# Performance work log

Measured on AMD Instinct MI355X. Metric: run time of the kernel, lower is better.

The kernel has to match this reference:

```python
import jax, jax.numpy as jnp
import numpy as np

V, D, H, DA, A, S = 50000, 512, 512, 128, 3, 512
MAXS = 8  # max stack depth reached by the generated action sequence
N_ACT = 768


def _lstm(x, h, c, Wih, Whh, bih, bhh):
    # torch.nn.LSTMCell math (batch of 1, vectors of shape (H,))
    z = Wih @ x + bih + Whh @ h + bhh
    i, f, g, o = jnp.split(z, 4)
    i = jax.nn.sigmoid(i); f = jax.nn.sigmoid(f); o = jax.nn.sigmoid(o)
    g = jnp.tanh(g)
    c2 = f * c + i * g
    return o * jnp.tanh(c2), c2


def _forward(sentence, actions, word_embeds, action_embeds, relation_embeds,
             empty_emb, h0, c0, Wih5, Whh5, bih5, bhh5,
             Wih_a, Whh_a, bih_a, bhh_a, W1, b1, W2, b2, We, be):
    # cell ids: 0=buffer 1=stack 2=output 3=entity_fwd 4=entity_bwd
    cell = lambda i, x, h, c: _lstm(x, h, c, Wih5[i], Whh5[i], bih5[i], bhh5[i])
    we = word_embeds[sentence]                      # (S, D) token reps (dropout = identity, eval)
    # buffer StackRNN: tokens pushed in reverse; precompute all buffer states once
    def bstep(hc, x):
        h2, c2 = cell(0, x, hc[0], hc[1])
        return (h2, c2), h2
    _, Hb = jax.lax.scan(bstep, (h0, c0), we[::-1])
    Hbuf = jnp.concatenate([h0[None], Hb], 0)       # (S+1, H); Hbuf[p] = top-of-buffer h at pointer p
    Hs = jnp.zeros((MAXS + 1, H), we.dtype).at[0].set(h0)
    Cs = jnp.zeros((MAXS + 1, H), we.dtype).at[0].set(c0)
    Tk = jnp.zeros((MAXS + 1, D), we.dtype)         # token stored with each stack entry

    def step(carry, a):
        pb, ps, po, pa, Hs, Cs, Tk, ho, co, ha, ca = carry
        buf_e = jnp.where(pb > 0, Hbuf[pb], empty_emb)
        stk_e = jnp.where(ps > 0, Hs[ps], empty_emb)
        out_e = jnp.where(po > 0, ho, empty_emb)
        act_e = jnp.where(pa > 0, ha, empty_emb)
        feat = jnp.concatenate([stk_e, buf_e, out_e, act_e])  # (4H,)
        logits = W2 @ jnp.tanh(W1 @ feat + b1) + b2           # (A,)
        nll = -jax.nn.log_softmax(logits)[a]
        tok_b = we[jnp.clip(S - pb, 0, S - 1)]                # top-of-buffer token
        # SHIFT candidate: push buffer token onto stack LSTM
        hs2, cs2 = cell(1, tok_b, Hs[ps], Cs[ps])
        # OUT candidate: push buffer token onto output LSTM
        ho_o, co_o = cell(2, tok_b, ho, co)
        # REDUCE candidate: pop stack entry, run entity fwd/bwd cells, compose, push to output
        tok_s = Tk[ps]
        ehf, _ = cell(3, tok_s, h0, c0)
        ehb, _ = cell(4, tok_s, h0, c0)
        ent = jnp.tanh(We @ jnp.concatenate([ehf, ehb, relation_embeds[a]]) + be)
        ho_r, co_r = cell(2, ent, ho, co)
        sh = a == 0; ot = a == 1; rd = a == 2
        w = jnp.clip(ps + 1, 0, MAXS)
        Hs = Hs.at[w].set(jnp.where(sh, hs2, Hs[w]))
        Cs = Cs.at[w].set(jnp.where(sh, cs2, Cs[w]))
        Tk = Tk.at[w].set(jnp.where(sh, tok_b, Tk[w]))
        ho = jnp.where(ot, ho_o, jnp.where(rd, ho_r, ho))
        co = jnp.where(ot, co_o, jnp.where(rd, co_r, co))
        ha, ca = _lstm(action_embeds[a], ha, ca, Wih_a, Whh_a, bih_a, bhh_a)
        pb = pb - jnp.where(sh | ot, 1, 0)
        ps = ps + jnp.where(sh, 1, 0) - jnp.where(rd, 1, 0)
        po = po + jnp.where(ot | rd, 1, 0)
        pa = pa + 1
        return (pb, ps, po, pa, Hs, Cs, Tk, ho, co, ha, ca), nll

    init = (jnp.int32(S), jnp.int32(0), jnp.int32(0), jnp.int32(0),
            Hs, Cs, Tk, h0, c0, h0, c0)
    _, nlls = jax.lax.scan(step, init, actions)
    return nlls  # (N_ACT,) per-action negative log-likelihoods


def setup_inputs() -> dict:
    key = jax.random.key(0)
    ks = jax.random.split(key, 24)
    f = lambda k, shp: jax.random.normal(k, shp, dtype=jnp.float32) * 0.05
    sentence = jax.random.randint(ks[0], (S,), 1, V, dtype=jnp.int32)
    # valid transition sequence: even token -> OUT; odd token -> SHIFT then REDUCE
    acts = []
    for i in range(S):
        acts += [1] if i % 2 == 0 else [0, 2]
    actions = jnp.asarray(np.array(acts, dtype=np.int32))
    return dict(
        sentence=sentence, actions=actions,
        word_embeds=f(ks[1], (V, D)),
        action_embeds=f(ks[2], (A, DA)),
        relation_embeds=f(ks[3], (A, DA)),
        empty_emb=f(ks[4], (H,)), h0=f(ks[5], (H,)), c0=f(ks[6], (H,)),
        Wih5=f(ks[7], (5, 4 * H, D)), Whh5=f(ks[8], (5, 4 * H, H)),
        bih5=f(ks[9], (5, 4 * H)), bhh5=f(ks[10], (5, 4 * H)),
        Wih_a=f(ks[11], (4 * H, DA)), Whh_a=f(ks[12], (4 * H, H)),
        bih_a=f(ks[13], (4 * H,)), bhh_a=f(ks[14], (4 * H,)),
        W1=f(ks[15], (H, 4 * H)), b1=f(ks[16], (H,)),
        W2=f(ks[17], (A, H)), b2=f(ks[18], (A,)),
        We=f(ks[19], (D, 2 * H + DA)), be=f(ks[20], (D,)))


def reference(sentence, actions, word_embeds, action_embeds, relation_embeds,
              empty_emb, h0, c0, Wih5, Whh5, bih5, bhh5,
              Wih_a, Whh_a, bih_a, bhh_a, W1, b1, W2, b2, We, be):
    return _forward(sentence, actions, word_embeds, action_embeds, relation_embeds,
                    empty_emb, h0, c0, Wih5, Whh5, bih5, bhh5,
                    Wih_a, Whh_a, bih_a, bhh_a, W1, b1, W2, b2, We, be)
```

## Files before the change

kernel.cpp:

```cpp
#include <hip/hip_runtime.h>
#include <math.h>

#define H 512
#define D 512
#define DA 128
#define MAXS 8
#define GH 2048
#define SFIX 512
#define NFIX 768
#define WPC 16
#define CANARY 0x7FC00BADu

typedef unsigned short ushort_t;

__device__ __forceinline__ float b2f(ushort_t v) {
  return __uint_as_float(((unsigned int)v) << 16);
}
__device__ __forceinline__ float sigm_f(float x) {
  return 1.f / (1.f + __expf(-x));
}
__device__ __forceinline__ float tanh_f(float x) {
  return 1.f - 2.f / (1.f + __expf(2.f * x));
}

__device__ int   g_dtype;
__device__ float g_Wih5[5 * GH * D];
__device__ float g_WihA[GH * DA];
__device__ float g_W1[H * GH];
__device__ float g_We[H * (2 * H + DA)];
__device__ float g_W2[3 * H];
__device__ float g_aemb[3 * DA];
__device__ float g_remb[3 * DA];
__device__ float g_empty[H];
__device__ float g_h0[H];
__device__ float g_c0[H];
__device__ float g_b1[H];
__device__ float g_be[D];
__device__ float g_b2[4];
__device__ float g_bih5[5 * GH];
__device__ float g_bhh5[5 * GH];
__device__ float g_bihA[GH];
__device__ float g_bhhA[GH];
__device__ int g_bidx_xb[SFIX];
__device__ int g_bsh[NFIX], g_csh[NFIX], g_par[NFIX], g_map_s[NFIX];
__device__ int g_bot[NFIX], g_cot[NFIX];
__device__ int g_bre[NFIX], g_cre[NFIX], g_map_o[NFIX];
__device__ int g_btok[NFIX], g_cide[NFIX], g_redact[NFIX];
__device__ int g_bufp[NFIX], g_stksrc[NFIX], g_outsrc[NFIX];
__device__ int g_counts[16];
__device__ float g_we[SFIX * D];
__device__ float g_cb[6 * GH];
__device__ float g_Pa[3 * GH];
__device__ float g_XB[SFIX * GH];
__device__ float g_Xso[NFIX * GH];
__device__ float g_E[NFIX * GH];
__device__ float g_E2[NFIX * GH];
__device__ float g_Bent[NFIX * 1152];
__device__ float g_ent[NFIX * H];
__device__ float g_Hbuf[(SFIX + 1) * H];
__device__ float g_Sh[NFIX * H], g_Sc[NFIX * H];
__device__ float g_Hos[NFIX * H], g_Has[NFIX * H];
__device__ float g_feat[NFIX * GH];
__device__ float g_t1[NFIX * H];

__device__ __forceinline__ float* f_conv(int s) {
  switch (s) {
    case 0: return g_Wih5;  case 1: return g_WihA;  case 2: return g_W1;
    case 3: return g_We;    case 4: return g_W2;    case 5: return g_aemb;
    case 6: return g_remb;  case 7: return g_empty; case 8: return g_h0;
    case 9: return g_c0;    case 10: return g_b1;   case 11: return g_be;
    case 12: return g_b2;   case 13: return g_bih5; case 14: return g_bhh5;
    case 15: return g_bihA; case 16: return g_bhhA;
    default: return nullptr;
  }
}
__device__ __forceinline__ const float* f_amat(int s) {
  switch (s) {
    case 0: return g_Wih5; case 1: return g_WihA;
    case 2: return g_We;   case 3: return g_W1;
    default: return nullptr;
  }
}
__device__ __forceinline__ const float* f_src(int s) {
  switch (s) {
    case 0: return g_we;   case 1: return g_ent; case 2: return g_Bent;
    case 3: return g_feat; case 4: return g_aemb;
    default: return nullptr;
  }
}
__device__ __forceinline__ float* f_dst(int s) {
  switch (s) {
    case 0: return g_Pa;  case 1: return g_XB;  case 2: return g_Xso;
    case 3: return g_E;   case 4: return g_ent; case 5: return g_t1;
    case 6: return g_E2;
    default: return nullptr;
  }
}
__device__ __forceinline__ const float* f_bias(int s) {
  switch (s) {
    case 0: return g_cb; case 1: return g_be; case 2: return g_b1;
    default: return nullptr;
  }
}
__device__ __forceinline__ const int* i_arr(int s) {
  switch (s) {
    case 0: return g_bidx_xb;
    case 1: return g_bsh;  case 2: return g_csh;
    case 3: return g_bot;  case 4: return g_cot;
    case 5: return g_bre;  case 6: return g_cre;
    case 7: return g_btok; case 8: return g_cide;
    default: return nullptr;
  }
}

__device__ __forceinline__ float lda_f(const float* p) {
  return __hip_atomic_load(p, __ATOMIC_RELAXED, __HIP_MEMORY_SCOPE_AGENT);
}
__device__ __forceinline__ void sta_f(float* p, float v) {
  __hip_atomic_store(p, v, __ATOMIC_RELAXED, __HIP_MEMORY_SCOPE_AGENT);
}
__device__ __forceinline__ float poll_f(const float* p) {
  float v = lda_f(p);
  while (__float_as_uint(v) == CANARY) {
    __builtin_amdgcn_s_sleep(1);
    v = lda_f(p);
  }
  return v;
}

__global__ void k_detect(const void* __restrict__ h0raw) {
  __shared__ int cnt;
  int t = threadIdx.x;
  if (t == 0) cnt = 0;
  __syncthreads();
  const ushort_t* u = (const ushort_t*)h0raw;
  if (t < 256) {
    ushort_t v = u[2 * t];
    int e = (v >> 7) & 0xFF;
    int ok = (e == 0) || (e >= 96 && e <= 134);
    atomicAdd(&cnt, ok);
  }
  __syncthreads();
  if (t == 0) g_dtype = (cnt >= 160) ? 1 : 0;
}

__global__ void k_poison() {
  const float pv = __uint_as_float(CANARY);
  size_t i = (size_t)blockIdx.x * blockDim.x + threadIdx.x;
  size_t stride = (size_t)gridDim.x * blockDim.x;
  for (size_t k = i; k < (size_t)(SFIX + 1) * H; k += stride) g_Hbuf[k] = pv;
  for (size_t k = i; k < (size_t)NFIX * H; k += stride) {
    g_Sh[k] = pv; g_Sc[k] = pv; g_Hos[k] = pv; g_Has[k] = pv;
  }
}

__global__ void k_b2f(const void* __restrict__ src, int dsel, int n) {
  float* dst = f_conv(dsel);
  int bf = g_dtype;
  int i = blockIdx.x * blockDim.x + threadIdx.x;
  int stride = gridDim.x * blockDim.x;
  if (bf) {
    const ushort_t* s = (const ushort_t*)src;
    for (; i < n; i += stride) dst[i] = b2f(s[i]);
  } else {
    const float* s = (const float*)src;
    for (; i < n; i += stride) dst[i] = s[i];
  }
}

__global__ void k_makewe(const int* __restrict__ sent, const void* __restrict__ wemb, int S) {
  int i = blockIdx.x;
  int tok = sent[i];
  if (tok < 0) tok = 0;
  float* dst = g_we + (size_t)i * D;
  if (g_dtype) {
    const ushort_t* src = (const ushort_t*)wemb + (size_t)tok * D;
    for (int j = threadIdx.x; j < D; j += blockDim.x) dst[j] = b2f(src[j]);
  } else {
    const float* src = (const float*)wemb + (size_t)tok * D;
    for (int j = threadIdx.x; j < D; j += blockDim.x) dst[j] = src[j];
  }
}

__global__ void k_traj(const int* __restrict__ actions, int NACT, int S) {
  int tid = threadIdx.x;
  for (int t = tid; t < NACT; t += blockDim.x) {
    g_bsh[t] = -1; g_csh[t] = -1; g_par[t] = -1; g_map_s[t] = 0;
    g_bot[t] = -1; g_cot[t] = -1;
    g_bre[t] = -1; g_cre[t] = -1; g_map_o[t] = 0;
    g_btok[t] = -1; g_cide[t] = -1; g_redact[t] = 0;
  }
  for (int t = tid; t < S; t += blockDim.x) g_bidx_xb[t] = S - 1 - t;
  __syncthreads();
  if (tid != 0) return;

  int pb = S, ps = 0, po = 0, nsh = 0, nred = 0;
  int slot_id[MAXS + 1], slot_tok[MAXS + 1];
  for (int s = 0; s <= MAXS; s++) { slot_id[s] = -2; slot_tok[s] = -1; }

  for (int t = 0; t < NACT; t++) {
    int a = actions[t];
    g_bufp[t] = pb;
    int rs = (ps < MAXS) ? ps : MAXS;
    g_stksrc[t] = (ps > 0) ? slot_id[rs] : -1;
    g_outsrc[t] = po;
    int tb = S - pb; if (tb < 0) tb = 0; if (tb > S - 1) tb = S - 1;
    if (a == 0) {
      g_par[nsh] = (ps == 0) ? -1 : slot_id[rs];
      g_map_s[nsh] = t;
      g_bsh[t] = tb; g_csh[t] = t;
      int w = (ps + 1 < MAXS) ? ps + 1 : MAXS;
      slot_id[w] = nsh; slot_tok[w] = tb;
      nsh++; ps++; pb--;
    } else if (a == 1) {
      g_bot[t] = tb; g_cot[t] = t;
      g_map_o[po] = t;
      po++; pb--;
    } else {
      g_btok[nred] = (ps > 0) ? slot_tok[rs] : -1;
      g_cide[nred] = nred; g_redact[nred] = (a < 0) ? 0 : ((a > 2) ? 2 : a);
      g_bre[t] = nred; g_cre[t] = t;
      g_map_o[po] = t;
      po++; nred++;
      ps = (ps > 0) ? ps - 1 : 0;
    }
    if (pb < 0) pb = 0;
  }
  g_counts[0] = nsh; g_counts[1] = po; g_counts[2] = nred;
}

__global__ void k_cbias(const void* __restrict__ Whh5raw) {
  int idx = blockIdx.x * blockDim.x + threadIdx.x;
  if (idx >= 6 * GH) return;
  int c = idx >> 11, m = idx & (GH - 1);
  float v;
  if (c < 5) v = g_bih5[c * GH + m] + g_bhh5[c * GH + m];
  else       v = g_bihA[m] + g_bhhA[m];
  if (c == 3 || c == 4) {
    size_t base = ((size_t)c * GH + m) * H;
    float acc = 0.f;
    if (g_dtype) {
      const ushort_t* w = (const ushort_t*)Whh5raw;
      for (int k = 0; k < H; k++) acc += b2f(w[base + k]) * g_h0[k];
    } else {
      const float* w = (const float*)Whh5raw;
      for (int k = 0; k < H; k++) acc += w[base + k] * g_h0[k];
    }
    v += acc;
  }
  g_cb[idx] = v;
}

__device__ void gemm_body(
    int asel, int aoff, int M, int K,
    int bsel, int bstride,
    int bidx_sel, int cidx_sel, int N,
    int bias_sel, int cb_off, int csel, int act,
    int bx, int by) {
  const float* A = f_amat(asel) + aoff;
  const float* Bsrc = f_src(bsel);
  const float* bias = f_bias(bias_sel) + cb_off;
  const int* bidx = i_arr(bidx_sel);
  const int* cidx = i_arr(cidx_sel);
  float* C = f_dst(csel);

  int mblk = bx * 64, nblk = by * 64;
  __shared__ int rowc[64];
  __shared__ float As[16][68];
  __shared__ float Bs[16][68];
  int tid = threadIdx.x;
  if (tid < 64) {
    int n = nblk + tid;
    int cr = -1;
    if (n < N) cr = cidx ? cidx[n] : n;
    if (cr >= NFIX) cr = -1;
    rowc[tid] = cr;
  }
  __syncthreads();
  bool any = false;
  for (int i = 0; i < 64; i++) if (rowc[i] >= 0) { any = true; break; }
  if (!any) return;

  float acc[4][4] = {};
  int tx = tid & 15, ty = tid >> 4;
  int mm = tid >> 2, kq = (tid & 3) * 4;
  int n = nblk + mm;
  const float* bp = nullptr;
  if (n < N) {
    if (bidx) { int bi = bidx[n]; if (bi >= 0 && bi < NFIX) bp = Bsrc + (size_t)bi * bstride; }
    else bp = Bsrc + (size_t)n * bstride;
  }
  const float* ap = A + (size_t)(mblk + mm) * K + kq;

  for (int k0 = 0; k0 < K; k0 += 16) {
    float4 av = *(const float4*)(ap + k0);
    float4 bv = bp ? *(const float4*)(bp + k0 + kq) : make_float4(0.f, 0.f, 0.f, 0.f);
    As[kq + 0][mm] = av.x; As[kq + 1][mm] = av.y; As[kq + 2][mm] = av.z; As[kq + 3][mm] = av.w;
    Bs[kq + 0][mm] = bv.x; Bs[kq + 1][mm] = bv.y; Bs[kq + 2][mm] = bv.z; Bs[kq + 3][mm] = bv.w;
    __syncthreads();
#pragma unroll
    for (int kk = 0; kk < 16; kk++) {
      float a0 = As[kk][tx * 4 + 0], a1 = As[kk][tx * 4 + 1];
      float a2 = As[kk][tx * 4 + 2], a3 = As[kk][tx * 4 + 3];
      float b0 = Bs[kk][ty * 4 + 0], b1 = Bs[kk][ty * 4 + 1];
      float b2 = Bs[kk][ty * 4 + 2], b3 = Bs[kk][ty * 4 + 3];
      acc[0][0] = fmaf(b0, a0, acc[0][0]); acc[0][1] = fmaf(b0, a1, acc[0][1]);
      acc[0][2] = fmaf(b0, a2, acc[0][2]); acc[0][3] = fmaf(b0, a3, acc[0][3]);
      acc[1][0] = fmaf(b1, a0, acc[1][0]); acc[1][1] = fmaf(b1, a1, acc[1][1]);
      acc[1][2] = fmaf(b1, a2, acc[1][2]); acc[1][3] = fmaf(b1, a3, acc[1][3]);
      acc[2][0] = fmaf(b2, a0, acc[2][0]); acc[2][1] = fmaf(b2, a1, acc[2][1]);
      acc[2][2] = fmaf(b2, a2, acc[2][2]); acc[2][3] = fmaf(b2, a3, acc[2][3]);
      acc[3][0] = fmaf(b3, a0, acc[3][0]); acc[3][1] = fmaf(b3, a1, acc[3][1]);
      acc[3][2] = fmaf(b3, a2, acc[3][2]); acc[3][3] = fmaf(b3, a3, acc[3][3]);
    }
    __syncthreads();
  }
#pragma unroll
  for (int i = 0; i < 4; i++) {
    int crow = rowc[ty * 4 + i];
    if (crow < 0) continue;
    int mj = mblk + tx * 4;
    float4 v;
    v.x = acc[i][0] + bias[mj + 0];
    v.y = acc[i][1] + bias[mj + 1];
    v.z = acc[i][2] + bias[mj + 2];
    v.w = acc[i][3] + bias[mj + 3];
    if (act) { v.x = tanh_f(v.x); v.y = tanh_f(v.y); v.z = tanh_f(v.z); v.w = tanh_f(v.w); }
    *(float4*)(C + (size_t)crow * M + mj) = v;
  }
}

__global__ __launch_bounds__(256) void k_gemm(
    int asel, int aoff, int M, int K,
    int bsel, int bstride,
    int bidx_sel, int cidx_sel, int N,
    int bias_sel, int cb_off, int csel, int act) {
  gemm_body(asel, aoff, M, K, bsel, bstride, bidx_sel, cidx_sel, N,
            bias_sel, cb_off, csel, act, blockIdx.x, blockIdx.y);
}

__global__ __launch_bounds__(256) void k_gemm_mega(
    int o1, int o2, int o3, int o4, int o5, int S, int NACT) {
  int bid = blockIdx.x;
  int job, base;
  if (bid < o1)      { job = 0; base = 0;  }
  else if (bid < o2) { job = 1; base = o1; }
  else if (bid < o3) { job = 2; base = o2; }
  else if (bid < o4) { job = 3; base = o3; }
  else if (bid < o5) { job = 4; base = o4; }
  else               { job = 5; base = o5; }
  int rel = bid - base, bx = rel & 31, by = rel >> 5;
  switch (job) {
    case 0: gemm_body(1, 0, GH, DA, 4, DA, -1, -1, 3, 0, 5 * GH, 0, 0, bx, by); break;
    case 1: gemm_body(0, 0, GH, D, 0, D, 0, -1, S, 0, 0, 1, 0, bx, by); break;
    case 2: gemm_body(0, 1 * GH * D, GH, D, 0, D, 1, 2, NACT, 0, GH, 2, 0, bx, by); break;
    case 3: gemm_body(0, 2 * GH * D, GH, D, 0, D, 3, 4, NACT, 0, 2 * GH, 2, 0, bx, by); break;
    case 4: gemm_body(0, 3 * GH * D, GH, D, 0, D, 7, 8, NACT, 0, 3 * GH, 3, 0, bx, by); break;
    case 5: gemm_body(0, 4 * GH * D, GH, D, 0, D, 7, 8, NACT, 0, 4 * GH, 6, 0, bx, by); break;
  }
}

__global__ void k_entityAB() {
  int r = blockIdx.x;
  if (g_cide[r] < 0) return;
  int j = threadIdx.x;
  const float* z = g_E + (size_t)r * GH;
  float c2 = sigm_f(z[j + 512]) * g_c0[j] + sigm_f(z[j]) * tanh_f(z[j + 1024]);
  g_Bent[(size_t)r * 1152 + j] = sigm_f(z[j + 1536]) * tanh_f(c2);
  const float* z2 = g_E2 + (size_t)r * GH;
  float c2b = sigm_f(z2[j + 512]) * g_c0[j] + sigm_f(z2[j]) * tanh_f(z2[j + 1024]);
  g_Bent[(size_t)r * 1152 + 512 + j] = sigm_f(z2[j + 1536]) * tanh_f(c2b);
  if (j < DA) g_Bent[(size_t)r * 1152 + 1024 + j] = g_remb[g_redact[r] * DA + j];
}

__global__ __launch_bounds__(512, 1) void k_chain_mw(
    const int* __restrict__ acts,
    const void* __restrict__ Whh5raw, const void* __restrict__ WhhAraw,
    int S, int NACT) {
  const int bid = blockIdx.x;
  const int chain = bid & 3;
  const int wslot = bid >> 2;
  const int j0 = wslot * 32;
  const int t = threadIdx.x;
  const int chunk = t >> 6;
  const int rl = t & 63;
  const int m0 = (rl >> 5) * 512 + j0 + (rl & 31);
  const int m1 = m0 + 1024;
  const int kb = chunk * 64;

  float* outH; int nsteps;
  if (chain == 0)      { outH = g_Hbuf + H; nsteps = S; }
  else if (chain == 1) { outH = g_Sh;       nsteps = g_counts[0]; }
  else if (chain == 2) { outH = g_Hos;      nsteps = g_counts[1]; }
  else                 { outH = g_Has;      nsteps = NACT; }
  if (nsteps > NFIX) nsteps = NFIX;

  float4 wv0[16], wv1[16];
  if (g_dtype) {
    const ushort_t* base = (chain < 3) ? (const ushort_t*)Whh5raw + (size_t)chain * GH * H
                                       : (const ushort_t*)WhhAraw;
    const ushort_t* p0 = base + (size_t)m0 * H + kb;
    const ushort_t* p1 = base + (size_t)m1 * H + kb;
#pragma unroll
    for (int i = 0; i < 16; i++) {
      ushort4 u0 = *(const ushort4*)(p0 + 4 * i);
      ushort4 u1 = *(const ushort4*)(p1 + 4 * i);
      wv0[i].x = b2f(u0.x); wv0[i].y = b2f(u0.y); wv0[i].z = b2f(u0.z); wv0[i].w = b2f(u0.w);
      wv1[i].x = b2f(u1.x); wv1[i].y = b2f(u1.y); wv1[i].z = b2f(u1.z); wv1[i].w = b2f(u1.w);
    }
  } else {
    const float* base = (chain < 3) ? (const float*)Whh5raw + (size_t)chain * GH * H
                                    : (const float*)WhhAraw;
    const float* p0 = base + (size_t)m0 * H + kb;
    const float* p1 = base + (size_t)m1 * H + kb;
#pragma unroll
    for (int i = 0; i < 16; i++) {
      wv0[i] = *(const float4*)(p0 + 4 * i);
      wv1[i] = *(const float4*)(p1 + 4 * i);
    }
  }

  __shared__ float4 hsh4[128];
  __shared__ float  psh[2][8][128];
  float creg = 0.f;
  if (chain != 1 && t < 32) creg = g_c0[j0 + t];

  for (int s = 0; s < nsteps; s++) {
    const float* xrow;
    if (chain == 0)      xrow = g_XB + (size_t)s * GH;
    else if (chain == 1) { int mm = g_map_s[s]; if (mm < 0) mm = 0; if (mm >= NFIX) mm = NFIX - 1;
                           xrow = g_Xso + (size_t)mm * GH; }
    else if (chain == 2) { int mm = g_map_o[s]; if (mm < 0) mm = 0; if (mm >= NFIX) mm = NFIX - 1;
                           xrow = g_Xso + (size_t)mm * GH; }
    else                 { int a = acts[s]; if (a < 0) a = 0; if (a > 2) a = 2;
                           xrow = g_Pa + (size_t)a * GH; }
    float xv0 = 0.f, xv1 = 0.f;
    if (chunk == 0) { xv0 = xrow[m0]; xv1 = xrow[m1]; }

    int pval = -1;
    const float* hp;
    if (chain == 1) {
      int p = g_par[s]; if (p >= NFIX) p = NFIX - 1;
      pval = p;
      hp = (p == -1) ? g_h0 : ((p < -1) ? nullptr : g_Sh + (size_t)p * H);
    } else {
      hp = (s == 0) ? g_h0 : outH + (size_t)(s - 1) * H;
    }
    const bool h_local = (chain != 1) ? (s == 0) : (pval == -1);

    {
      float v;
      if (h_local)          v = hp[t];
      else if (hp == nullptr) v = 0.f;
      else                  v = poll_f(hp + t);
      ((float*)hsh4)[t] = v;
    }
    asm volatile("s_waitcnt lgkmcnt(0)" ::: "memory");
    __builtin_amdgcn_sched_barrier(0);

    float4 a0 = make_float4(0.f, 0.f, 0.f, 0.f);
    float4 a1 = make_float4(0.f, 0.f, 0.f, 0.f);
#pragma unroll
    for (int i = 0; i < 16; i++) {
      float4 hv = hsh4[(chunk << 4) + i];
      a0.x = fmaf(wv0[i].x, hv.x, a0.x);
      a0.y = fmaf(wv0[i].y, hv.y, a0.y);
      a0.z = fmaf(wv0[i].z, hv.z, a0.z);
      a0.w = fmaf(wv0[i].w, hv.w, a0.w);
      a1.x = fmaf(wv1[i].x, hv.x, a1.x);
      a1.y = fmaf(wv1[i].y, hv.y, a1.y);
      a1.z = fmaf(wv1[i].z, hv.z, a1.z);
      a1.w = fmaf(wv1[i].w, hv.w, a1.w);
    }
    float pp0 = (a0.x + a0.y) + (a0.z + a0.w);
    float pp1 = (a1.x + a1.y) + (a1.z + a1.w);
    if (chunk == 0) { pp0 += xv0; pp1 += xv1; }
    const int pp = s & 1;
    psh[pp][chunk][rl] = pp0;
    psh[pp][chunk][rl + 64] = pp1;
    __syncthreads();

    if (t < 32) {
      float zi = 0.f, zf = 0.f, zg = 0.f, zo = 0.f;
#pragma unroll
      for (int c = 0; c < 8; c++) {
        zi += psh[pp][c][t];
        zf += psh[pp][c][32 + t];
        zg += psh[pp][c][64 + t];
        zo += psh[pp][c][96 + t];
      }
      float i_ = sigm_f(zi);
      float f_ = sigm_f(zf);
      float o_ = sigm_f(zo);
      int j = j0 + t;
      float cprev;
      if (chain == 1) {
        if (pval == -1)      cprev = g_c0[j];
        else if (pval < -1)  cprev = 0.f;
        else                 cprev = poll_f(&g_Sc[(size_t)pval * H + j]);
      } else {
        cprev = creg;
      }
      float c2 = f_ * cprev + i_ * tanh_f(zg);
      float hn = o_ * tanh_f(c2);
      if (chain == 1) sta_f(&g_Sc[(size_t)s * H + j], c2);
      else            creg = c2;
      sta_f(&outH[(size_t)s * H + j], hn);
    }
  }
}

__global__ void k_feat() {
  int t = blockIdx.x;
  int j = threadIdx.x;
  float* f = g_feat + (size_t)t * GH;
  int s = g_stksrc[t]; if (s >= NFIX) s = NFIX - 1;
  f[j] = (s == -1) ? g_empty[j] : ((s < 0) ? 0.f : g_Sh[(size_t)s * H + j]);
  int p = g_bufp[t]; if (p > SFIX) p = SFIX;
  f[H + j] = (p > 0) ? g_Hbuf[(size_t)p * H + j] : g_empty[j];
  int k = g_outsrc[t]; if (k > NFIX) k = NFIX;
  f[2 * H + j] = (k > 0) ? g_Hos[(size_t)(k - 1) * H + j] : g_empty[j];
  f[3 * H + j] = (t > 0) ? g_Has[(size_t)(t - 1) * H + j] : g_empty[j];
}

__global__ void k_final(const int* __restrict__ actions, void* __restrict__ out) {
  int t = blockIdx.x;
  int lane = threadIdx.x;
  const float* tv = g_t1 + (size_t)t * H;
  float a0 = 0.f, a1 = 0.f, a2 = 0.f;
  for (int j = lane; j < H; j += 64) {
    float v = tv[j];
    a0 += g_W2[j] * v; a1 += g_W2[H + j] * v; a2 += g_W2[2 * H + j] * v;
  }
  for (int off = 32; off; off >>= 1) {
    a0 += __shfl_down(a0, off);
    a1 += __shfl_down(a1, off);
    a2 += __shfl_down(a2, off);
  }
  if (lane == 0) {
    a0 += g_b2[0]; a1 += g_b2[1]; a2 += g_b2[2];
    float m = fmaxf(a0, fmaxf(a1, a2));
    float lse = m + logf(expf(a0 - m) + expf(a1 - m) + expf(a2 - m));
    int a = actions[t];
    float la = (a <= 0) ? a0 : ((a == 1) ? a1 : a2);
    float v = lse - la;
    if (g_dtype) {
      unsigned int b = __float_as_uint(v);
      b += 0x7FFFu + ((b >> 16) & 1u);
      ((ushort_t*)out)[t] = (ushort_t)(b >> 16);
    } else {
      ((float*)out)[t] = v;
    }
  }
}

extern "C" void kernel_launch(void* const* d_in, const int* in_sizes, int n_in,
                              void* d_out, int out_size, void* d_ws, size_t ws_size,
                              hipStream_t stream) {
  const int* sent   = (const int*)d_in[0];
  const int* actions= (const int*)d_in[1];
  const void* wemb  = d_in[2];
  const void* aemb  = d_in[3];
  const void* remb  = d_in[4];
  const void* empty = d_in[5];
  const void* h0    = d_in[6];
  const void* c0    = d_in[7];
  const void* Wih5  = d_in[8];
  const void* Whh5  = d_in[9];
  const void* bih5  = d_in[10];
  const void* bhh5  = d_in[11];
  const void* Wih_a = d_in[12];
  const void* Whh_a = d_in[13];
  const void* bih_a = d_in[14];
  const void* bhh_a = d_in[15];
  const void* W1    = d_in[16];
  const void* b1    = d_in[17];
  const void* W2    = d_in[18];
  const void* b2    = d_in[19];
  const void* We    = d_in[20];
  const void* be    = d_in[21];
  int S = in_sizes[0];
  int NACT = in_sizes[1];
  if (S > SFIX) S = SFIX;
  if (NACT > NFIX) NACT = NFIX;
  (void)n_in; (void)out_size; (void)d_ws; (void)ws_size;

  k_detect<<<1, 256, 0, stream>>>(h0);
  k_poison<<<1024, 256, 0, stream>>>();

  auto conv = [&](const void* src, int dsel, int n) {
    int blocks = (n + 255) / 256; if (blocks > 1024) blocks = 1024;
    k_b2f<<<blocks, 256, 0, stream>>>(src, dsel, n);
  };
  conv(Wih5, 0, 5 * GH * D);
  conv(Wih_a, 1, GH * DA);
  conv(W1, 2, H * GH);
  conv(We, 3, H * (2 * H + DA));
  conv(W2, 4, 3 * H);
  conv(aemb, 5, 3 * DA);
  conv(remb, 6, 3 * DA);
  conv(empty, 7, H);
  conv(h0, 8, H);
  conv(c0, 9, H);
  conv(b1, 10, H);
  conv(be, 11, D);
  conv(b2, 12, 3);
  conv(bih5, 13, 5 * GH);
  conv(bhh5, 14, 5 * GH);
  conv(bih_a, 15, GH);
  conv(bhh_a, 16, GH);

  k_makewe<<<S, 256, 0, stream>>>(sent, wemb, S);
  k_traj<<<1, 64, 0, stream>>>(actions, NACT, S);
  k_cbias<<<(6 * GH + 255) / 256, 256, 0, stream>>>(Whh5);

  int gyS = (S + 63) / 64, gyN = (NACT + 63) / 64;
  int o1 = 32;
  int o2 = o1 + 32 * gyS;
  int o3 = o2 + 32 * gyN;
  int o4 = o3 + 32 * gyN;
  int o5 = o4 + 32 * gyN;
  int total = o5 + 32 * gyN;
  k_gemm_mega<<<total, 256, 0, stream>>>(o1, o2, o3, o4, o5, S, NACT);
  k_entityAB<<<NACT, 512, 0, stream>>>();

  dim3 gN(GH / 64, gyN);
  dim3 gH(H / 64, gyN);
  k_gemm<<<gH, 256, 0, stream>>>(2, 0, H, 2 * H + DA, 2, 1152, -1, 8, NACT, 1, 0, 4, 1);
  k_gemm<<<gN, 256, 0, stream>>>(0, 2 * GH * D, GH, D, 1, H, 5, 6, NACT, 0, 2 * GH, 2, 0);
  k_chain_mw<<<64, 512, 0, stream>>>(actions, Whh5, Whh_a, S, NACT);
  k_feat<<<NACT, 512, 0, stream>>>();
  k_gemm<<<gH, 256, 0, stream>>>(3, 0, H, GH, 3, GH, -1, -1, NACT, 2, 0, 5, 1);
  k_final<<<NACT, 64, 0, stream>>>(actions, d_out);
}
```

Before: 1.954 ms.

## Make each wave own whole hidden units to remove block barrier in recurrence

```diff
diff --git a/kernel.cpp b/kernel.cpp
--- a/kernel.cpp
+++ b/kernel.cpp
@@ -127,6 +127,9 @@
   }
   return v;
 }
+__device__ __forceinline__ void pin4(float4& v) {
+  asm volatile("" : "+v"(v.x), "+v"(v.y), "+v"(v.z), "+v"(v.w));
+}
 
 __global__ void k_detect(const void* __restrict__ h0raw) {
   __shared__ int cnt;
@@ -382,11 +385,15 @@
   const int wslot = bid >> 2;
   const int j0 = wslot * 32;
   const int t = threadIdx.x;
-  const int chunk = t >> 6;
-  const int rl = t & 63;
-  const int m0 = (rl >> 5) * 512 + j0 + (rl & 31);
-  const int m1 = m0 + 1024;
-  const int kb = chunk * 64;
+  const int w = t >> 6;
+  const int l = t & 63;
+  const int g = l >> 4;
+  const int jj = (l >> 2) & 3;
+  const int kseg = l & 3;
+  const int j = j0 + 4 * w + jj;
+  const int m = g * 512 + j;
+  const int kb = kseg * 128;
+  const int sl = (l & 3) * 4;
 
   float* outH; int nsteps;
   if (chain == 0)      { outH = g_Hbuf + H; nsteps = S; }
@@ -395,35 +402,34 @@
   else                 { outH = g_Has;      nsteps = NACT; }
   if (nsteps > NFIX) nsteps = NFIX;
 
-  float4 wv0[16], wv1[16];
+  float4 wv[32];
   if (g_dtype) {
     const ushort_t* base = (chain < 3) ? (const ushort_t*)Whh5raw + (size_t)chain * GH * H
                                        : (const ushort_t*)WhhAraw;
-    const ushort_t* p0 = base + (size_t)m0 * H + kb;
-    const ushort_t* p1 = base + (size_t)m1 * H + kb;
+    const ushort_t* p0 = base + (size_t)m * H + kb;
 #pragma unroll
-    for (int i = 0; i < 16; i++) {
-      ushort4 u0 = *(const ushort4*)(p0 + 4 * i);
-      ushort4 u1 = *(const ushort4*)(p1 + 4 * i);
-      wv0[i].x = b2f(u0.x); wv0[i].y = b2f(u0.y); wv0[i].z = b2f(u0.z); wv0[i].w = b2f(u0.w);
-      wv1[i].x = b2f(u1.x); wv1[i].y = b2f(u1.y); wv1[i].z = b2f(u1.z); wv1[i].w = b2f(u1.w);
+    for (int i = 0; i < 32; i++) {
+      ushort4 u = *(const ushort4*)(p0 + 4 * i);
+      wv[i].x = b2f(u.x); wv[i].y = b2f(u.y); wv[i].z = b2f(u.z); wv[i].w = b2f(u.w);
     }
   } else {
     const float* base = (chain < 3) ? (const float*)Whh5raw + (size_t)chain * GH * H
                                     : (const float*)WhhAraw;
-    const float* p0 = base + (size_t)m0 * H + kb;
-    const float* p1 = base + (size_t)m1 * H + kb;
+    const float* p0 = base + (size_t)m * H + kb;
 #pragma unroll
-    for (int i = 0; i < 16; i++) {
-      wv0[i] = *(const float4*)(p0 + 4 * i);
-      wv1[i] = *(const float4*)(p1 + 4 * i);
-    }
-  }
-
-  __shared__ float4 hsh4[128];
-  __shared__ float  psh[2][8][128];
+    for (int i = 0; i < 32; i++) wv[i] = *(const float4*)(p0 + 4 * i);
+  }
+#pragma unroll
+  for (int i = 0; i < 32; i++) pin4(wv[i]);
+
+  __shared__ __align__(16) float hw[8][4 * 132];
   float creg = 0.f;
-  if (chain != 1 && t < 32) creg = g_c0[j0 + t];
+  if (chain != 1 && l < 4) creg = g_c0[j0 + 4 * w + l];
+
+  const int poff = 8 * l;
+  const int wchunk = l >> 4;
+  float* wdst = &hw[w][wchunk * 132 + 8 * (l & 15)];
+  const float* hrd = &hw[w][kseg * 132];
 
   for (int s = 0; s < nsteps; s++) {
     const float* xrow;
@@ -434,8 +440,7 @@
                            xrow = g_Xso + (size_t)mm * GH; }
     else                 { int a = acts[s]; if (a < 0) a = 0; if (a > 2) a = 2;
                            xrow = g_Pa + (size_t)a * GH; }
-    float xv0 = 0.f, xv1 = 0.f;
-    if (chunk == 0) { xv0 = xrow[m0]; xv1 = xrow[m1]; }
+    float xv = (kseg == 0) ? xrow[m] : 0.f;
 
     int pval = -1;
     const float* hp;
@@ -448,64 +453,64 @@
     }
     const bool h_local = (chain != 1) ? (s == 0) : (pval == -1);
 
-    {
-      float v;
-      if (h_local)          v = hp[t];
-      else if (hp == nullptr) v = 0.f;
-      else                  v = poll_f(hp + t);
-      ((float*)hsh4)[t] = v;
-    }
+    float v0, v1, v2, v3, v4, v5, v6, v7;
+    if (h_local) {
+      const float* hb = hp + poff;
+      v0 = hb[0]; v1 = hb[1]; v2 = hb[2]; v3 = hb[3];
+      v4 = hb[4]; v5 = hb[5]; v6 = hb[6]; v7 = hb[7];
+    } else if (hp == nullptr) {
+      v0 = v1 = v2 = v3 = v4 = v5 = v6 = v7 = 0.f;
+    } else {
+      const float* hb = hp + poff;
+      for (;;) {
+        v0 = lda_f(hb + 0); v1 = lda_f(hb + 1); v2 = lda_f(hb + 2); v3 = lda_f(hb + 3);
+        v4 = lda_f(hb + 4); v5 = lda_f(hb + 5); v6 = lda_f(hb + 6); v7 = lda_f(hb + 7);
+        unsigned bad = (__float_as_uint(v0) == CANARY) | (__float_as_uint(v1) == CANARY)
+                     | (__float_as_uint(v2) == CANARY) | (__float_as_uint(v3) == CANARY)
+                     | (__float_as_uint(v4) == CANARY) | (__float_as_uint(v5) == CANARY)
+                     | (__float_as_uint(v6) == CANARY) | (__float_as_uint(v7) == CANARY);
+        if (!bad) break;
+        __builtin_amdgcn_s_sleep(1);
+      }
+    }
+    *(float4*)wdst = make_float4(v0, v1, v2, v3);
+    *(float4*)(wdst + 4) = make_float4(v4, v5, v6, v7);
     asm volatile("s_waitcnt lgkmcnt(0)" ::: "memory");
     __builtin_amdgcn_sched_barrier(0);
 
-    float4 a0 = make_float4(0.f, 0.f, 0.f, 0.f);
-    float4 a1 = make_float4(0.f, 0.f, 0.f, 0.f);
+    float4 a4 = make_float4(0.f, 0.f, 0.f, 0.f);
 #pragma unroll
-    for (int i = 0; i < 16; i++) {
-      float4 hv = hsh4[(chunk << 4) + i];
-      a0.x = fmaf(wv0[i].x, hv.x, a0.x);
-      a0.y = fmaf(wv0[i].y, hv.y, a0.y);
-      a0.z = fmaf(wv0[i].z, hv.z, a0.z);
-      a0.w = fmaf(wv0[i].w, hv.w, a0.w);
-      a1.x = fmaf(wv1[i].x, hv.x, a1.x);
-      a1.y = fmaf(wv1[i].y, hv.y, a1.y);
-      a1.z = fmaf(wv1[i].z, hv.z, a1.z);
-      a1.w = fmaf(wv1[i].w, hv.w, a1.w);
-    }
-    float pp0 = (a0.x + a0.y) + (a0.z + a0.w);
-    float pp1 = (a1.x + a1.y) + (a1.z + a1.w);
-    if (chunk == 0) { pp0 += xv0; pp1 += xv1; }
-    const int pp = s & 1;
-    psh[pp][chunk][rl] = pp0;
-    psh[pp][chunk][rl + 64] = pp1;
-    __syncthreads();
-
-    if (t < 32) {
-      float zi = 0.f, zf = 0.f, zg = 0.f, zo = 0.f;
-#pragma unroll
-      for (int c = 0; c < 8; c++) {
-        zi += psh[pp][c][t];
-        zf += psh[pp][c][32 + t];
-        zg += psh[pp][c][64 + t];
-        zo += psh[pp][c][96 + t];
-      }
-      float i_ = sigm_f(zi);
-      float f_ = sigm_f(zf);
-      float o_ = sigm_f(zo);
-      int j = j0 + t;
+    for (int i = 0; i < 32; i++) {
+      float4 hv = *(const float4*)(hrd + 4 * i);
+      a4.x = fmaf(wv[i].x, hv.x, a4.x);
+      a4.y = fmaf(wv[i].y, hv.y, a4.y);
+      a4.z = fmaf(wv[i].z, hv.z, a4.z);
+      a4.w = fmaf(wv[i].w, hv.w, a4.w);
+    }
+    float z = (a4.x + a4.y) + (a4.z + a4.w) + xv;
+    z += __shfl_xor(z, 1);
+    z += __shfl_xor(z, 2);
+    float av = (g == 2) ? tanh_f(z) : sigm_f(z);
+    float gi = __shfl(av, sl);
+    float gf = __shfl(av, 16 + sl);
+    float gg = __shfl(av, 32 + sl);
+    float go = __shfl(av, 48 + sl);
+
+    if (l < 4) {
+      int jg = j0 + 4 * w + l;
       float cprev;
       if (chain == 1) {
-        if (pval == -1)      cprev = g_c0[j];
+        if (pval == -1)      cprev = g_c0[jg];
         else if (pval < -1)  cprev = 0.f;
-        else                 cprev = poll_f(&g_Sc[(size_t)pval * H + j]);
+        else                 cprev = poll_f(&g_Sc[(size_t)pval * H + jg]);
       } else {
         cprev = creg;
       }
-      float c2 = f_ * cprev + i_ * tanh_f(zg);
-      float hn = o_ * tanh_f(c2);
-      if (chain == 1) sta_f(&g_Sc[(size_t)s * H + j], c2);
+      float c2 = gf * cprev + gi * gg;
+      float hn = go * tanh_f(c2);
+      if (chain == 1) sta_f(&g_Sc[(size_t)s * H + jg], c2);
       else            creg = c2;
-      sta_f(&outH[(size_t)s * H + j], hn);
+      sta_f(&outH[(size_t)s * H + jg], hn);
     }
   }
 }
```

Measured after the change: 4.483 ms. +129.4%, slower.
